# Performance work log

Measured on AMD Instinct MI355X. Metric: run time of the kernel, lower is better.

## Reference

```python
import jax, jax.numpy as jnp
import numpy as np
import math

B, S, E, H, FF = 2, 2048, 1024, 16, 4096
HD = E // H
EPS = 1e-6


def layer_norm(x, gamma, beta):
    mu = jnp.mean(x, axis=-1, keepdims=True)
    var = jnp.mean(jnp.square(x - mu), axis=-1, keepdims=True)
    return (x - mu) * jax.lax.rsqrt(var + EPS) * gamma + beta


def setup_inputs() -> dict:
    key = jax.random.key(0)
    ks = jax.random.split(key, 8)
    x_embeds = jax.random.normal(ks[0], (B, S, E), dtype=jnp.float32)
    # causal mask: True means masked (j > i), broadcastable over batch/heads
    mask = jnp.triu(jnp.ones((S, S), dtype=bool), k=1)[None, None]
    sc = 1.0 / math.sqrt(E)
    w_kqv = jax.random.normal(ks[1], (3 * E, E), dtype=jnp.float32) * sc
    w_o = jax.random.normal(ks[2], (E, E), dtype=jnp.float32) * sc
    w_up = jax.random.normal(ks[3], (FF, E), dtype=jnp.float32) * sc
    b_up = jnp.zeros((FF,), dtype=jnp.float32)
    w_down = jax.random.normal(ks[4], (E, FF), dtype=jnp.float32) / math.sqrt(FF)
    b_down = jnp.zeros((E,), dtype=jnp.float32)
    g1 = jnp.ones((E,), dtype=jnp.float32)
    b1 = jnp.zeros((E,), dtype=jnp.float32)
    g2 = jnp.ones((E,), dtype=jnp.float32)
    b2 = jnp.zeros((E,), dtype=jnp.float32)
    return {"x_embeds": x_embeds, "mask": mask, "w_kqv": w_kqv, "w_o": w_o,
            "w_up": w_up, "b_up": b_up, "w_down": w_down, "b_down": b_down,
            "g1": g1, "b1": b1, "g2": g2, "b2": b2}


def reference(x_embeds, mask, w_kqv, w_o, w_up, b_up, w_down, b_down, g1, b1, g2, b2):
    b, s = x_embeds.shape[0], x_embeds.shape[1]
    # --- attention ---
    kqv = x_embeds @ w_kqv.T                      # [B,S,3E]
    kqv = kqv.reshape(b, s, 3, H, HD).transpose(0, 3, 2, 1, 4)  # [B,H,3,S,HD]
    xk, xq, xv = kqv[:, :, 0], kqv[:, :, 1], kqv[:, :, 2]
    attn = jnp.einsum('bhqd,bhkd->bhqk', xq, xk) / math.sqrt(HD)
    attn = jnp.where(mask, -jnp.inf, attn)
    attn = jax.nn.softmax(attn, axis=-1)
    out = jnp.einsum('bhqk,bhkd->bhqd', attn, xv)  # [B,H,S,HD]
    out = out.transpose(0, 2, 1, 3).reshape(b, s, E)
    out = out @ w_o.T
    x = layer_norm(out + x_embeds, g1, b1)
    # --- ffnn ---
    h = jax.nn.relu(x @ w_up.T + b_up)
    h = h @ w_down.T + b_down
    return layer_norm(h + x, g2, b2)
```

## Files before the change

### kernel.cpp

```cpp
#include <hip/hip_runtime.h>
#include <stdint.h>

#define B_ 2
#define S_ 2048
#define E_ 1024
#define H_ 16
#define HD_ 64
#define FF_ 4096
#define M_ 4096
#define LOG2E_ 1.44269504f

typedef short bf16x8 __attribute__((ext_vector_type(8)));
typedef float f32x4  __attribute__((ext_vector_type(4)));
typedef short shortx4 __attribute__((ext_vector_type(4)));

#define MFMA16(a,b,c) __builtin_amdgcn_mfma_f32_16x16x32_bf16(a,b,c,0,0,0)

__device__ __forceinline__ short f2bf(float f) {
  uint32_t u = __builtin_bit_cast(uint32_t, f);
  u += 0x7fffu + ((u >> 16) & 1u);
  return (short)(u >> 16);
}
__device__ __forceinline__ float bf2f(short b) {
  uint32_t u = ((uint32_t)(uint16_t)b) << 16;
  return __builtin_bit_cast(float, u);
}
__device__ __forceinline__ float exp2_hw(float x) {
  float r;
  asm("v_exp_f32 %0, %1" : "=v"(r) : "v"(x));
  return r;
}

template<int CTRL>
__device__ __forceinline__ float dpp_ror(float x) {
  return __builtin_bit_cast(float,
    __builtin_amdgcn_update_dpp(0, __builtin_bit_cast(int, x), CTRL, 0xF, 0xF, true));
}
__device__ __forceinline__ float dpp_max16(float v) {
  v = fmaxf(v, dpp_ror<0x128>(v));
  v = fmaxf(v, dpp_ror<0x124>(v));
  v = fmaxf(v, dpp_ror<0x122>(v));
  v = fmaxf(v, dpp_ror<0x121>(v));
  return v;
}
__device__ __forceinline__ float dpp_sum16(float v) {
  v += dpp_ror<0x128>(v);
  v += dpp_ror<0x124>(v);
  v += dpp_ror<0x122>(v);
  v += dpp_ror<0x121>(v);
  return v;
}

#define GLDS16(g, l) __builtin_amdgcn_global_load_lds( \
    (const __attribute__((address_space(1))) unsigned int*)(g), \
    (__attribute__((address_space(3))) unsigned int*)(l), 16, 0, 0)

__global__ void cast_all(const float* __restrict__ x, const float* __restrict__ wkqv,
                         const float* __restrict__ wo, const float* __restrict__ wup,
                         const float* __restrict__ wdown,
                         short* __restrict__ xb, short* __restrict__ wkqvb,
                         short* __restrict__ wob, short* __restrict__ wupb,
                         short* __restrict__ wdownb) {
  const int stride = gridDim.x * blockDim.x;
  for (int i = blockIdx.x * blockDim.x + threadIdx.x; i < 4194304; i += stride) {
    const int e = i << 2;
    const float* src; short* dst; int off;
    if (e < 4194304)       { src = x;     dst = xb;     off = e; }
    else if (e < 7340032)  { src = wkqv;  dst = wkqvb;  off = e - 4194304; }
    else if (e < 8388608)  { src = wo;    dst = wob;    off = e - 7340032; }
    else if (e < 12582912) { src = wup;   dst = wupb;   off = e - 8388608; }
    else                   { src = wdown; dst = wdownb; off = e - 12582912; }
    float4 v = *(const float4*)(src + off);
    shortx4 o;
    o.x = f2bf(v.x); o.y = f2bf(v.y); o.z = f2bf(v.z); o.w = f2bf(v.w);
    *(shortx4*)(dst + off) = o;
  }
}

template<int SK, int EPI, typename OutT>
__global__ __launch_bounds__(256) void gemm_bt(
    const short* __restrict__ A, const short* __restrict__ Bw,
    OutT* __restrict__ C0, OutT* __restrict__ C1, const float* __restrict__ bias,
    int M, int N, int K)
{
  __shared__ short Al[2][128 * 32];
  __shared__ short Bl[2][128 * 32];
  const int tid  = threadIdx.x;
  const int w    = tid >> 6, lane = tid & 63;
  const int ntiles = N >> 7;
  const int nwg = gridDim.x;
  const int bid = blockIdx.x;
  const int swz = (bid & 7) * (nwg >> 3) + (bid >> 3);
  const int tn = swz % ntiles, tm = swz / ntiles;
  const int m0 = tm << 7, n0 = tn << 7;
  const int wr = (w >> 1) << 6, wc = (w & 1) << 6;
  const int lr = lane & 15, lk = (lane >> 4) << 3;
  const int ra = lane >> 2, colA = (lane & 3) << 3;

  const int kper = K / SK;
  const int kbeg = (SK > 1) ? (int)blockIdx.y * kper : 0;
  const int T = kper >> 5;
  OutT* __restrict__ C = (SK > 1 && blockIdx.y) ? C1 : C0;

  const short* Ag0 = A  + (size_t)(m0 + w * 16 + ra) * K + colA;
  const short* Ag1 = A  + (size_t)(m0 + (w + 4) * 16 + ra) * K + colA;
  const short* Bg0 = Bw + (size_t)(n0 + w * 16 + ra) * K + colA;
  const short* Bg1 = Bw + (size_t)(n0 + (w + 4) * 16 + ra) * K + colA;

  f32x4 acc[4][4] = {};

  {
    const int k0 = kbeg;
    GLDS16(Ag0 + k0, &Al[0][w * 512]);
    GLDS16(Ag1 + k0, &Al[0][(w + 4) * 512]);
    GLDS16(Bg0 + k0, &Bl[0][w * 512]);
    GLDS16(Bg1 + k0, &Bl[0][(w + 4) * 512]);
  }

  for (int it = 0; it < T; ++it) {
    const int buf = it & 1;
    if (it + 1 < T) {
      const int k1 = kbeg + ((it + 1) << 5);
      GLDS16(Ag0 + k1, &Al[buf ^ 1][w * 512]);
      GLDS16(Ag1 + k1, &Al[buf ^ 1][(w + 4) * 512]);
      GLDS16(Bg0 + k1, &Bl[buf ^ 1][w * 512]);
      GLDS16(Bg1 + k1, &Bl[buf ^ 1][(w + 4) * 512]);
      asm volatile("s_waitcnt vmcnt(4)" ::: "memory");
    } else {
      asm volatile("s_waitcnt vmcnt(0)" ::: "memory");
    }
    __builtin_amdgcn_sched_barrier(0);
    __builtin_amdgcn_s_barrier();

    bf16x8 af[4], bfr[4];
    #pragma unroll
    for (int i = 0; i < 4; ++i)
      af[i] = *(const bf16x8*)&Al[buf][(wr + i * 16 + lr) * 32 + lk];
    #pragma unroll
    for (int j = 0; j < 4; ++j)
      bfr[j] = *(const bf16x8*)&Bl[buf][(wc + j * 16 + lr) * 32 + lk];
    #pragma unroll
    for (int i = 0; i < 4; ++i)
      #pragma unroll
      for (int j = 0; j < 4; ++j)
        acc[i][j] = MFMA16(af[i], bfr[j], acc[i][j]);

    __builtin_amdgcn_s_barrier();
  }

  const int lg = lane >> 4;
  #pragma unroll
  for (int j = 0; j < 4; ++j) {
    const int col = n0 + wc + j * 16 + lr;
    float bv = 0.f;
    if constexpr (SK == 1 && EPI != 0) bv = bias[col];
    #pragma unroll
    for (int i = 0; i < 4; ++i) {
      #pragma unroll
      for (int r = 0; r < 4; ++r) {
        const int row = m0 + wr + i * 16 + lg * 4 + r;
        float v = acc[i][j][r] + bv;
        if constexpr (SK == 1 && EPI == 1) v = fmaxf(v, 0.f);
        if constexpr (sizeof(OutT) == 2) C[(size_t)row * N + col] = f2bf(v);
        else                             C[(size_t)row * N + col] = v;
      }
    }
  }
}

__global__ __launch_bounds__(512) void attn_kernel(
    const short* __restrict__ kqv, short* __restrict__ out)
{
  __shared__ short Kt[64][72];
  __shared__ short Vt[64][72];
  __shared__ short Pl[8][16][72];

  const int tid = threadIdx.x, w = tid >> 6, lane = tid & 63;
  const int wt = w & 3;
  const int p = blockIdx.x;
  const int bh = blockIdx.y;
  const int b = bh >> 4, h = bh & 15;
  const int q0 = ((w < 4) ? (31 - p) : p) << 6;
  const int nkb = 32 - p;
  const int lr = lane & 15, lg = lane >> 4;

  const size_t rowq = (size_t)(b * S_ + q0 + wt * 16 + lr) * 3072 + 1024 + h * 64;
  bf16x8 qf[2];
  qf[0] = *(const bf16x8*)&kqv[rowq + lg * 8];
  qf[1] = *(const bf16x8*)&kqv[rowq + 32 + lg * 8];
  #pragma unroll
  for (int ks = 0; ks < 2; ++ks)
    #pragma unroll
    for (int e = 0; e < 8; ++e)
      qf[ks][e] = f2bf(bf2f(qf[ks][e]) * 0.125f);

  f32x4 acc[4] = {};
  float m_run[4], l_run[4];
  #pragma unroll
  for (int r = 0; r < 4; ++r) { m_run[r] = -1e30f; l_run[r] = 0.f; }

  const int skk = tid >> 3;
  const int sc  = (tid & 7) << 3;
  const int vws = (tid & 7) << 3;

  for (int kbi = 0; kbi < nkb; ++kbi) {
    const int kb = kbi << 6;
    {
      const size_t gb = (size_t)(b * S_ + kb + skk) * 3072 + h * 64 + sc;
      *(bf16x8*)&Kt[skk][sc] = *(const bf16x8*)&kqv[gb];
      bf16x8 vv = *(const bf16x8*)&kqv[gb + 2048];
      const int kc = skk ^ vws;
      #pragma unroll
      for (int e = 0; e < 8; ++e) Vt[sc + e][kc] = vv[e];
    }
    __syncthreads();

    if (kb <= q0 + wt * 16 + 15) {
      f32x4 sacc[4] = {};
      __builtin_amdgcn_s_setprio(1);
      #pragma unroll
      for (int jt = 0; jt < 4; ++jt) {
        #pragma unroll
        for (int ks = 0; ks < 2; ++ks) {
          bf16x8 kf = *(const bf16x8*)&Kt[jt * 16 + lr][ks * 32 + lg * 8];
          sacc[jt] = MFMA16(qf[ks], kf, sacc[jt]);
        }
      }
      __builtin_amdgcn_s_setprio(0);
      const bool full = (kb + 63 <= q0 + wt * 16);
      float rmax[4];
      if (full) {
        #pragma unroll
        for (int r = 0; r < 4; ++r)
          rmax[r] = fmaxf(fmaxf(sacc[0][r], sacc[1][r]), fmaxf(sacc[2][r], sacc[3][r]));
      } else {
        #pragma unroll
        for (int r = 0; r < 4; ++r) rmax[r] = -1e30f;
        #pragma unroll
        for (int jt = 0; jt < 4; ++jt) {
          const int kpos = kb + jt * 16 + lr;
          #pragma unroll
          for (int r = 0; r < 4; ++r) {
            const int qrow = q0 + wt * 16 + lg * 4 + r;
            float v = (kpos <= qrow) ? sacc[jt][r] : -1e30f;
            sacc[jt][r] = v;
            rmax[r] = fmaxf(rmax[r], v);
          }
        }
      }
      #pragma unroll
      for (int r = 0; r < 4; ++r) rmax[r] = dpp_max16(rmax[r]);
      int need = 0;
      #pragma unroll
      for (int r = 0; r < 4; ++r) need |= (rmax[r] > m_run[r] + 8.f) ? 1 : 0;
      if (__any(need)) {
        #pragma unroll
        for (int r = 0; r < 4; ++r) {
          const float mn = fmaxf(m_run[r], rmax[r]);
          const float al = exp2_hw((m_run[r] - mn) * LOG2E_);
          m_run[r] = mn;
          l_run[r] *= al;
          #pragma unroll
          for (int dt = 0; dt < 4; ++dt) acc[dt][r] *= al;
        }
      }
      float m2[4], rsum[4];
      #pragma unroll
      for (int r = 0; r < 4; ++r) { m2[r] = m_run[r] * LOG2E_; rsum[r] = 0.f; }
      #pragma unroll
      for (int jt = 0; jt < 4; ++jt)
        #pragma unroll
        for (int r = 0; r < 4; ++r) {
          const float pv = exp2_hw(__builtin_fmaf(sacc[jt][r], LOG2E_, -m2[r]));
          sacc[jt][r] = pv;
          rsum[r] += pv;
        }
      #pragma unroll
      for (int r = 0; r < 4; ++r) { rsum[r] = dpp_sum16(rsum[r]); l_run[r] += rsum[r]; }
      #pragma unroll
      for (int jt = 0; jt < 4; ++jt) {
        uint32_t w01, w23;
        asm("v_cvt_pk_bf16_f32 %0, %1, %2" : "=v"(w01) : "v"(sacc[jt][0]), "v"(sacc[jt][1]));
        asm("v_cvt_pk_bf16_f32 %0, %1, %2" : "=v"(w23) : "v"(sacc[jt][2]), "v"(sacc[jt][3]));
        Pl[w][lg * 4 + 0][jt * 16 + lr] = (short)(w01 & 0xffffu);
        Pl[w][lg * 4 + 1][jt * 16 + lr] = (short)(w01 >> 16);
        Pl[w][lg * 4 + 2][jt * 16 + lr] = (short)(w23 & 0xffffu);
        Pl[w][lg * 4 + 3][jt * 16 + lr] = (short)(w23 >> 16);
      }
      bf16x8 pa[2];
      pa[0] = *(const bf16x8*)&Pl[w][lr][lg * 8];
      pa[1] = *(const bf16x8*)&Pl[w][lr][32 + lg * 8];
      __builtin_amdgcn_s_setprio(1);
      #pragma unroll
      for (int dt = 0; dt < 4; ++dt) {
        const int vswz = (2 * dt + (lr >> 3)) << 3;
        #pragma unroll
        for (int ks = 0; ks < 2; ++ks) {
          bf16x8 vb = *(const bf16x8*)&Vt[dt * 16 + lr][(ks * 32 + lg * 8) ^ vswz];
          acc[dt] = MFMA16(pa[ks], vb, acc[dt]);
        }
      }
      __builtin_amdgcn_s_setprio(0);
    }
    __syncthreads();
  }

  #pragma unroll
  for (int dt = 0; dt < 4; ++dt) {
    #pragma unroll
    for (int r = 0; r < 4; ++r) {
      const int d = h * 64 + dt * 16 + lr;
      const int q_row = q0 + wt * 16 + lg * 4 + r;
      out[(size_t)(b * S_ + q_row) * E_ + d] = f2bf(acc[dt][r] / l_run[r]);
    }
  }
}

template<int FINAL>
__global__ __launch_bounds__(256) void ln_kernel(
    const float* __restrict__ y0, const float* __restrict__ y1,
    const float* __restrict__ bias, const void* __restrict__ res,
    const float* __restrict__ gam, const float* __restrict__ bet,
    void* __restrict__ outp)
{
  const int row = blockIdx.x, tid = threadIdx.x, lane = tid & 63, w = tid >> 6;
  float4 a = ((const float4*)(y0 + (size_t)row * E_))[tid];
  float4 c = ((const float4*)(y1 + (size_t)row * E_))[tid];
  float r[4] = {a.x + c.x, a.y + c.y, a.z + c.z, a.w + c.w};
  if constexpr (FINAL) {
    float4 bi = ((const float4*)bias)[tid];
    shortx4 rb = ((const shortx4*)((const short*)res + (size_t)row * E_))[tid];
    r[0] += bi.x + bf2f(rb.x); r[1] += bi.y + bf2f(rb.y);
    r[2] += bi.z + bf2f(rb.z); r[3] += bi.w + bf2f(rb.w);
  } else {
    float4 rv = ((const float4*)((const float*)res + (size_t)row * E_))[tid];
    r[0] += rv.x; r[1] += rv.y; r[2] += rv.z; r[3] += rv.w;
  }
  float s  = r[0] + r[1] + r[2] + r[3];
  float ss = r[0]*r[0] + r[1]*r[1] + r[2]*r[2] + r[3]*r[3];
  #pragma unroll
  for (int m = 32; m >= 1; m >>= 1) { s += __shfl_xor(s, m); ss += __shfl_xor(ss, m); }
  __shared__ float red[8];
  if (lane == 0) { red[w] = s; red[4 + w] = ss; }
  __syncthreads();
  s  = red[0] + red[1] + red[2] + red[3];
  ss = red[4] + red[5] + red[6] + red[7];
  const float mu  = s * (1.f / E_);
  const float var = ss * (1.f / E_) - mu * mu;
  const float rs  = rsqrtf(var + 1e-6f);
  float4 gv = ((const float4*)gam)[tid];
  float4 bv = ((const float4*)bet)[tid];
  float o0 = (r[0] - mu) * rs * gv.x + bv.x;
  float o1 = (r[1] - mu) * rs * gv.y + bv.y;
  float o2 = (r[2] - mu) * rs * gv.z + bv.z;
  float o3 = (r[3] - mu) * rs * gv.w + bv.w;
  if constexpr (FINAL) {
    float4 o; o.x = o0; o.y = o1; o.z = o2; o.w = o3;
    ((float4*)((float*)outp + (size_t)row * E_))[tid] = o;
  } else {
    shortx4 o; o.x = f2bf(o0); o.y = f2bf(o1); o.z = f2bf(o2); o.w = f2bf(o3);
    ((shortx4*)((short*)outp + (size_t)row * E_))[tid] = o;
  }
}

extern "C" void kernel_launch(void* const* d_in, const int* in_sizes, int n_in,
                              void* d_out, int out_size, void* d_ws, size_t ws_size,
                              hipStream_t stream) {
  const float* x      = (const float*)d_in[0];
  const float* w_kqv  = (const float*)d_in[2];
  const float* w_o    = (const float*)d_in[3];
  const float* w_up   = (const float*)d_in[4];
  const float* b_up   = (const float*)d_in[5];
  const float* w_down = (const float*)d_in[6];
  const float* b_down = (const float*)d_in[7];
  const float* g1     = (const float*)d_in[8];
  const float* b1     = (const float*)d_in[9];
  const float* g2     = (const float*)d_in[10];
  const float* b2     = (const float*)d_in[11];
  float* out = (float*)d_out;

  char* ws = (char*)d_ws;
  short* xb     = (short*)(ws);
  short* wkqvb  = (short*)(ws + ((size_t)8  << 20));
  short* wob    = (short*)(ws + ((size_t)14 << 20));
  short* wupb   = (short*)(ws + ((size_t)16 << 20));
  short* wdownb = (short*)(ws + ((size_t)24 << 20));
  short* kqv    = (short*)(ws + ((size_t)32 << 20));
  float* proj0  = (float*)(ws + ((size_t)32 << 20));
  float* proj1  = (float*)(ws + ((size_t)48 << 20));
  short* hbuf   = (short*)(ws + ((size_t)32 << 20));
  short* attno  = (short*)(ws + ((size_t)64 << 20));
  short* xln    = (short*)(ws + ((size_t)72 << 20));
  float* down0  = (float*)(ws);
  float* down1  = (float*)(ws + ((size_t)80 << 20));

  cast_all<<<2048, 256, 0, stream>>>(x, w_kqv, w_o, w_up, w_down,
                                     xb, wkqvb, wob, wupb, wdownb);

  gemm_bt<1, 0, short><<<24 * 32, 256, 0, stream>>>(xb, wkqvb, kqv, nullptr, nullptr, M_, 3 * E_, E_);
  attn_kernel<<<dim3(16, B_ * H_), 512, 0, stream>>>(kqv, attno);
  gemm_bt<2, 0, float><<<dim3(256, 2), 256, 0, stream>>>(attno, wob, proj0, proj1, nullptr, M_, E_, E_);
  ln_kernel<0><<<M_, 256, 0, stream>>>(proj0, proj1, nullptr, x, g1, b1, xln);
  gemm_bt<1, 1, short><<<32 * 32, 256, 0, stream>>>(xln, wupb, hbuf, nullptr, b_up, M_, FF_, E_);
  gemm_bt<2, 0, float><<<dim3(256, 2), 256, 0, stream>>>(hbuf, wdownb, down0, down1, nullptr, M_, E_, FF_);
  ln_kernel<1><<<M_, 256, 0, stream>>>(down0, down1, b_down, xln, g2, b2, out);
}
```

Measured before the change: 252.5 us.

## Double-buffer K/V tiles in attention to overlap global loads with compute

The attention kernel now keeps two LDS buffers for K and V. It issues the global loads for the next key block into registers before computing the current block, then writes them to the alternate buffer afterwards. This removes one of the two barriers per iteration and hides global load latency behind the MFMA and softmax work. In exchange it doubles the K/V shared memory and holds the prefetched vectors in registers across the compute, which may reduce occupancy.

```diff
diff --git a/kernel.cpp b/kernel.cpp
--- a/kernel.cpp
+++ b/kernel.cpp
@@ -171,8 +171,8 @@
 __global__ __launch_bounds__(512) void attn_kernel(
     const short* __restrict__ kqv, short* __restrict__ out)
 {
-  __shared__ short Kt[64][72];
-  __shared__ short Vt[64][72];
+  __shared__ short Kt[2][64][72];
+  __shared__ short Vt[2][64][72];
   __shared__ short Pl[8][16][72];
 
   const int tid = threadIdx.x, w = tid >> 6, lane = tid & 63;
@@ -202,18 +202,29 @@
   const int skk = tid >> 3;
   const int sc  = (tid & 7) << 3;
   const int vws = (tid & 7) << 3;
+  const int vkc = skk ^ vws;
+  const short* gstage = kqv + (size_t)b * S_ * 3072 + h * 64 + sc;
+
+  {
+    bf16x8 kreg = *(const bf16x8*)&gstage[(size_t)skk * 3072];
+    bf16x8 vreg = *(const bf16x8*)&gstage[(size_t)skk * 3072 + 2048];
+    *(bf16x8*)&Kt[0][skk][sc] = kreg;
+    #pragma unroll
+    for (int e = 0; e < 8; ++e) Vt[0][sc + e][vkc] = vreg[e];
+  }
+  __syncthreads();
 
   for (int kbi = 0; kbi < nkb; ++kbi) {
+    const int buf = kbi & 1;
     const int kb = kbi << 6;
-    {
-      const size_t gb = (size_t)(b * S_ + kb + skk) * 3072 + h * 64 + sc;
-      *(bf16x8*)&Kt[skk][sc] = *(const bf16x8*)&kqv[gb];
-      bf16x8 vv = *(const bf16x8*)&kqv[gb + 2048];
-      const int kc = skk ^ vws;
-      #pragma unroll
-      for (int e = 0; e < 8; ++e) Vt[sc + e][kc] = vv[e];
-    }
-    __syncthreads();
+
+    bf16x8 kreg, vreg;
+    const bool more = (kbi + 1 < nkb);
+    if (more) {
+      const size_t gb = (size_t)(((kbi + 1) << 6) + skk) * 3072;
+      kreg = *(const bf16x8*)&gstage[gb];
+      vreg = *(const bf16x8*)&gstage[gb + 2048];
+    }
 
     if (kb <= q0 + wt * 16 + 15) {
       f32x4 sacc[4] = {};
@@ -222,7 +233,7 @@
       for (int jt = 0; jt < 4; ++jt) {
         #pragma unroll
         for (int ks = 0; ks < 2; ++ks) {
-          bf16x8 kf = *(const bf16x8*)&Kt[jt * 16 + lr][ks * 32 + lg * 8];
+          bf16x8 kf = *(const bf16x8*)&Kt[buf][jt * 16 + lr][ks * 32 + lg * 8];
           sacc[jt] = MFMA16(qf[ks], kf, sacc[jt]);
         }
       }
@@ -296,11 +307,17 @@
         const int vswz = (2 * dt + (lr >> 3)) << 3;
         #pragma unroll
         for (int ks = 0; ks < 2; ++ks) {
-          bf16x8 vb = *(const bf16x8*)&Vt[dt * 16 + lr][(ks * 32 + lg * 8) ^ vswz];
+          bf16x8 vb = *(const bf16x8*)&Vt[buf][dt * 16 + lr][(ks * 32 + lg * 8) ^ vswz];
           acc[dt] = MFMA16(pa[ks], vb, acc[dt]);
         }
       }
       __builtin_amdgcn_s_setprio(0);
+    }
+
+    if (more) {
+      *(bf16x8*)&Kt[buf ^ 1][skk][sc] = kreg;
+      #pragma unroll
+      for (int e = 0; e < 8; ++e) Vt[buf ^ 1][sc + e][vkc] = vreg[e];
     }
     __syncthreads();
   }
```

New measurement: 243.0 us. 1.04x faster.
